# Kernel optimization log

Hardware: AMD Instinct MI355X
Metric: run time of the kernel (lower is better)

Reference implementation:

```python
import jax, jax.numpy as jnp
import numpy as np

LOG2 = 0.6931471805599453

def ssp(x):
    # ShiftedSoftplus: softplus(x) - log(2)
    return jax.nn.softplus(x) - jnp.asarray(LOG2, x.dtype)

def setup_inputs() -> dict:
    key = jax.random.key(0)
    ks = jax.random.split(key, 12)
    B, N, D, F, R, P = 1, 50000, 128, 128, 20, 1600000
    s = lambda fan_in: 1.0 / np.sqrt(fan_in)
    return {
        "x": jax.random.normal(ks[0], (B, N, D), jnp.float32),
        "f_ij": jax.random.uniform(ks[1], (P, R), jnp.float32),
        "idx_i": jax.random.randint(ks[2], (P,), 0, B * N),
        "idx_j": jax.random.randint(ks[3], (P,), 0, B * N),
        "rcut_ij": jax.random.uniform(ks[4], (P,), jnp.float32),
        "W_in": jax.random.uniform(ks[5], (F, D), jnp.float32, -s(D), s(D)),
        "b_in": jax.random.uniform(ks[6], (F,), jnp.float32, -s(D), s(D)),
        "W_filter": jax.random.uniform(ks[7], (F, R), jnp.float32, -s(R), s(R)),
        "b_filter": jax.random.uniform(ks[8], (F,), jnp.float32, -s(R), s(R)),
        "W_out": jax.random.uniform(ks[9], (D, F), jnp.float32, -s(F), s(F)),
        "b_out": jax.random.uniform(ks[10], (D,), jnp.float32, -s(F), s(F)),
    }

def reference(x, f_ij, idx_i, idx_j, rcut_ij, W_in, b_in, W_filter, b_filter, W_out, b_out):
    B, N, _ = x.shape
    # input_to_feature: Linear(nr_atom_basis -> nr_filters)
    h = jnp.einsum('bnd,fd->bnf', x, W_in) + b_in          # [B,N,F]
    h = h.reshape(B * N, -1)                                # [B*N,F]
    # filter network: Linear(nr_rbf -> nr_filters) + ShiftedSoftplus, scaled by cutoff
    Wij = ssp(jnp.einsum('pr,fr->pf', f_ij, W_filter) + b_filter) * rcut_ij[:, None]  # [P,F]
    # gather -> mul -> scatter_add
    x_ij = h[idx_j] * Wij                                   # [P,F]
    agg = jax.ops.segment_sum(x_ij, idx_i, num_segments=B * N)  # [B*N,F]
    # feature_to_output: Linear(nr_filters -> nr_atom_basis) + ShiftedSoftplus
    out = ssp(jnp.einsum('nf,df->nd', agg, W_out) + b_out)  # [B*N,D]
    return out.reshape(B, N, 128)
```

## Files before the change

kernel.cpp:

```cpp
#include <hip/hip_runtime.h>
#include <hip/hip_bf16.h>

static constexpr float kLog2 = 0.6931471805599453f;

__device__ __forceinline__ float sspf(float x) {
    return fmaxf(x, 0.0f) + __logf(1.0f + __expf(-fabsf(x))) - kLog2;
}

typedef __attribute__((ext_vector_type(8))) _Float16 half8;
typedef __attribute__((ext_vector_type(4))) _Float16 half4v;
typedef __attribute__((ext_vector_type(4))) float float4v;

template <bool ACT, typename OUT>
__device__ __forceinline__ void gemm_mfma_body(const float* __restrict__ A,
                                               const float* __restrict__ B,
                                               const float* __restrict__ bias,
                                               OUT* __restrict__ C, int M,
                                               int blockid) {
    constexpr int LDH = 136;
    __shared__ _Float16 Als[64 * LDH];
    __shared__ _Float16 Bls[128 * LDH];
    const int tid = threadIdx.x;
    const int rowbase = blockid * 64;
#pragma unroll
    for (int j = 0; j < 8; ++j) {
        int idx = j * 256 + tid;
        int r = idx >> 5, c4 = (idx & 31) << 2;
        int rg = rowbase + r;
        rg = rg < M ? rg : (M - 1);
        float4 v = *(const float4*)(A + (size_t)rg * 128 + c4);
        half4v hv = {(_Float16)v.x, (_Float16)v.y, (_Float16)v.z, (_Float16)v.w};
        *(half4v*)&Als[r * LDH + c4] = hv;
    }
#pragma unroll
    for (int j = 0; j < 16; ++j) {
        int idx = j * 256 + tid;
        int r = idx >> 5, c4 = (idx & 31) << 2;
        float4 v = *(const float4*)(B + (size_t)r * 128 + c4);
        half4v hv = {(_Float16)v.x, (_Float16)v.y, (_Float16)v.z, (_Float16)v.w};
        *(half4v*)&Bls[r * LDH + c4] = hv;
    }
    __syncthreads();

    const int wave = tid >> 6, lane = tid & 63;
    const int l15 = lane & 15, q = lane >> 4;
    float4v acc[8];
#pragma unroll
    for (int nt = 0; nt < 8; ++nt) acc[nt] = (float4v){0.f, 0.f, 0.f, 0.f};
    const int am = wave * 16 + l15;
#pragma unroll
    for (int kk = 0; kk < 4; ++kk) {
        half8 af = *(const half8*)&Als[am * LDH + kk * 32 + q * 8];
#pragma unroll
        for (int nt = 0; nt < 8; ++nt) {
            half8 bf = *(const half8*)&Bls[(nt * 16 + l15) * LDH + kk * 32 + q * 8];
            acc[nt] = __builtin_amdgcn_mfma_f32_16x16x32_f16(af, bf, acc[nt], 0, 0, 0);
        }
    }
#pragma unroll
    for (int nt = 0; nt < 8; ++nt) {
        int n = nt * 16 + l15;
        float bv = bias[n];
#pragma unroll
        for (int r = 0; r < 4; ++r) {
            int m = rowbase + wave * 16 + q * 4 + r;
            if (m < M) {
                float v = acc[nt][r] + bv;
                if (ACT) v = sspf(v);
                C[(size_t)m * 128 + n] = (OUT)v;
            }
        }
    }
}

__global__ __launch_bounds__(256) void gemm_in_count_kernel(
    const float* __restrict__ A, const float* __restrict__ B,
    const float* __restrict__ bias, _Float16* __restrict__ C, int M,
    const int* __restrict__ idx_i, int* __restrict__ counts, int P,
    int gemm_blocks) {
    if ((int)blockIdx.x < gemm_blocks) {
        gemm_mfma_body<false, _Float16>(A, B, bias, C, M, blockIdx.x);
    } else {
        const int nthr = (gridDim.x - gemm_blocks) * 256;
        for (int p = (blockIdx.x - gemm_blocks) * 256 + threadIdx.x; p < P;
             p += nthr)
            atomicAdd(&counts[idx_i[p]], 1);
    }
}

__global__ __launch_bounds__(256) void gemm_out_kernel(
    const float* __restrict__ A, const float* __restrict__ B,
    const float* __restrict__ bias, float* __restrict__ C, int M) {
    gemm_mfma_body<true, float>(A, B, bias, C, M, blockIdx.x);
}

__global__ __launch_bounds__(256) void block_sums_kernel(
    const int* __restrict__ counts, int* __restrict__ partials, int N) {
    __shared__ int red[256];
    int t = threadIdx.x, g = blockIdx.x * 256 + t;
    red[t] = g < N ? counts[g] : 0;
    __syncthreads();
    for (int o = 128; o > 0; o >>= 1) {
        if (t < o) red[t] += red[t + o];
        __syncthreads();
    }
    if (t == 0) partials[blockIdx.x] = red[0];
}

__global__ __launch_bounds__(256) void scan_partials_kernel(int* __restrict__ partials,
                                                            int NB) {
    __shared__ int s[256];
    int t = threadIdx.x;
    s[t] = t < NB ? partials[t] : 0;
    __syncthreads();
    for (int o = 1; o < 256; o <<= 1) {
        int v = t >= o ? s[t - o] : 0;
        __syncthreads();
        s[t] += v;
        __syncthreads();
    }
    partials[t] = t ? s[t - 1] : 0;
}

__global__ __launch_bounds__(256) void write_offsets_kernel(
    const int* __restrict__ counts, const int* __restrict__ partials,
    int* __restrict__ offsets, int* __restrict__ cursor, int N) {
    __shared__ int s[256];
    int t = threadIdx.x, g = blockIdx.x * 256 + t;
    int c = g < N ? counts[g] : 0;
    s[t] = c;
    __syncthreads();
    for (int o = 1; o < 256; o <<= 1) {
        int v = t >= o ? s[t - o] : 0;
        __syncthreads();
        s[t] += v;
        __syncthreads();
    }
    int excl = partials[blockIdx.x] + s[t] - c;
    if (g < N) {
        offsets[g] = excl;
        cursor[g] = excl;
        if (g == N - 1) offsets[N] = excl + c;
    }
}

__global__ __launch_bounds__(256) void fill_kernel(const int* __restrict__ idx_i,
                                                   int* __restrict__ cursor,
                                                   int* __restrict__ csr, int P) {
    int p = blockIdx.x * 256 + threadIdx.x;
    if (p < P) {
        int pos = atomicAdd(&cursor[idx_i[p]], 1);
        csr[pos] = p;
    }
}

__global__ __launch_bounds__(256) void gather_mfma_kernel(
    const float* __restrict__ f_ij, const int* __restrict__ idx_j,
    const float* __restrict__ rcut, const float* __restrict__ Wf,
    const float* __restrict__ bf, const _Float16* __restrict__ h16,
    const int* __restrict__ offsets, const int* __restrict__ csr,
    float* __restrict__ agg, int N) {
    const int lane = threadIdx.x & 63;
    const int gwave = (blockIdx.x * 256 + threadIdx.x) >> 6;
    const int nwaves = (gridDim.x * 256) >> 6;
    const int l15 = lane & 15, q = lane >> 4;

    half8 wfr[8];
#pragma unroll
    for (int nt = 0; nt < 8; ++nt) {
        const float* wr = Wf + (size_t)(nt * 16 + l15) * 20;
        float v[8];
#pragma unroll
        for (int j = 0; j < 8; ++j) {
            int k = q * 8 + j;
            v[j] = (k < 20) ? wr[k] : ((k == 20) ? bf[nt * 16 + l15] : 0.0f);
        }
        wfr[nt] = (half8){(_Float16)v[0], (_Float16)v[1], (_Float16)v[2],
                          (_Float16)v[3], (_Float16)v[4], (_Float16)v[5],
                          (_Float16)v[6], (_Float16)v[7]};
    }
    const float4v zero = {0.f, 0.f, 0.f, 0.f};

    for (int i = gwave; i < N; i += nwaves) {
        const int s = __builtin_amdgcn_readfirstlane(offsets[i]);
        const int e = __builtin_amdgcn_readfirstlane(offsets[i + 1]);
        float4v acc[8];
#pragma unroll
        for (int nt = 0; nt < 8; ++nt) acc[nt] = zero;

        for (int c = s; c < e; c += 16) {
            const int k = c + l15;
            const int pidx = k < e ? k : (e - 1);
            const int p = csr[pidx];
            const int jb = idx_j[p] << 7;
            const float rc = (k < e) ? rcut[p] : 0.0f;
            const float* fp = f_ij + (size_t)p * 20;
            float b0 = 0.f, b1 = 0.f, b2 = 0.f, b3 = 0.f;
            float b4 = 0.f, b5 = 0.f, b6 = 0.f, b7 = 0.f;
            if (q <= 2) {
                float4 a = *(const float4*)(fp + q * 8);
                b0 = a.x; b1 = a.y; b2 = a.z; b3 = a.w;
            }
            if (q <= 1) {
                float4 bb = *(const float4*)(fp + q * 8 + 4);
                b4 = bb.x; b5 = bb.y; b6 = bb.z; b7 = bb.w;
            }
            if (q == 2) b4 = 1.0f;
            half8 bfrag = (half8){(_Float16)b0, (_Float16)b1, (_Float16)b2,
                                  (_Float16)b3, (_Float16)b4, (_Float16)b5,
                                  (_Float16)b6, (_Float16)b7};
#pragma unroll
            for (int nt = 0; nt < 8; ++nt) {
                float4v d = __builtin_amdgcn_mfma_f32_16x16x32_f16(wfr[nt], bfrag,
                                                                   zero, 0, 0, 0);
                half4v hv = *(const half4v*)(h16 + jb + nt * 16 + q * 4);
#pragma unroll
                for (int r = 0; r < 4; ++r) {
                    float w = sspf(d[r]) * rc;
                    acc[nt][r] = fmaf(w, (float)hv[r], acc[nt][r]);
                }
            }
        }
#pragma unroll
        for (int m = 1; m <= 8; m <<= 1)
#pragma unroll
            for (int nt = 0; nt < 8; ++nt)
#pragma unroll
                for (int r = 0; r < 4; ++r)
                    acc[nt][r] += __shfl_xor(acc[nt][r], m, 64);
        if (l15 == 0) {
#pragma unroll
            for (int nt = 0; nt < 8; ++nt) {
                float4 o = {acc[nt][0], acc[nt][1], acc[nt][2], acc[nt][3]};
                *(float4*)(agg + (size_t)i * 128 + nt * 16 + q * 4) = o;
            }
        }
    }
}

extern "C" void kernel_launch(void* const* d_in, const int* in_sizes, int n_in,
                              void* d_out, int out_size, void* d_ws, size_t ws_size,
                              hipStream_t stream) {
    const float* x     = (const float*)d_in[0];
    const float* f_ij  = (const float*)d_in[1];
    const int*   idx_i = (const int*)d_in[2];
    const int*   idx_j = (const int*)d_in[3];
    const float* rcut  = (const float*)d_in[4];
    const float* W_in  = (const float*)d_in[5];
    const float* b_in  = (const float*)d_in[6];
    const float* W_f   = (const float*)d_in[7];
    const float* b_f   = (const float*)d_in[8];
    const float* W_out = (const float*)d_in[9];
    const float* b_out = (const float*)d_in[10];

    const int N = in_sizes[0] / 128;
    const int P = in_sizes[2];
    const int NB = (N + 255) / 256;

    char* ws = (char*)d_ws;
    int* counts   = (int*)ws;  ws += ((size_t)N + 64) * 4;
    int* offsets  = (int*)ws;  ws += ((size_t)N + 64) * 4;
    int* cursor   = (int*)ws;  ws += ((size_t)N + 64) * 4;
    int* partials = (int*)ws;  ws += 1024;
    int* csr      = (int*)ws;  ws += (size_t)P * 4;
    _Float16* h16 = (_Float16*)ws;

    float* agg = (float*)d_out;

    const int mblocks = (N + 63) / 64;
    const int cblocks = 768;

    hipMemsetAsync(counts, 0, (size_t)N * 4, stream);
    gemm_in_count_kernel<<<mblocks + cblocks, 256, 0, stream>>>(
        x, W_in, b_in, h16, N, idx_i, counts, P, mblocks);
    block_sums_kernel<<<NB, 256, 0, stream>>>(counts, partials, N);
    scan_partials_kernel<<<1, 256, 0, stream>>>(partials, NB);
    write_offsets_kernel<<<NB, 256, 0, stream>>>(counts, partials, offsets, cursor, N);
    fill_kernel<<<(P + 255) / 256, 256, 0, stream>>>(idx_i, cursor, csr, P);
    gather_mfma_kernel<<<2048, 256, 0, stream>>>(f_ij, idx_j, rcut, W_f, b_f,
                                                 h16, offsets, csr, agg, N);
    gemm_out_kernel<<<mblocks, 256, 0, stream>>>(agg, W_out, b_out, (float*)d_out, N);
}
```

Measured before the change: 765.3 us.

## Replace three-kernel scan with atomic segment allocation and pre-sorted edge features

The three-kernel prefix scan is replaced by a single kernel that scans counts within each block and reserves each block's range with an atomic on a global total. Segment starts are therefore not in node order, which is valid for CSR grouping. The fill kernel now writes the edge payload in sorted order: packed idx_j and rcut, plus fp16 f_ij padded to 24 with the bias-one column when workspace allows. The gather kernel then reads contiguous data instead of indirecting through csr into f_ij, idx_j and rcut, and it prefetches the next chunk's metadata. This trades an extra scattered write pass of about 56 bytes per edge in fill for contiguous reads in the gather.

After: 628.4 us. 17.9% less time.

```diff
diff --git a/kernel.cpp b/kernel.cpp
--- a/kernel.cpp
+++ b/kernel.cpp
@@ -53,8 +53,8 @@
         half8 af = *(const half8*)&Als[am * LDH + kk * 32 + q * 8];
 #pragma unroll
         for (int nt = 0; nt < 8; ++nt) {
-            half8 bf = *(const half8*)&Bls[(nt * 16 + l15) * LDH + kk * 32 + q * 8];
-            acc[nt] = __builtin_amdgcn_mfma_f32_16x16x32_f16(af, bf, acc[nt], 0, 0, 0);
+            half8 bfv = *(const half8*)&Bls[(nt * 16 + l15) * LDH + kk * 32 + q * 8];
+            acc[nt] = __builtin_amdgcn_mfma_f32_16x16x32_f16(af, bfv, acc[nt], 0, 0, 0);
         }
     }
 #pragma unroll
@@ -94,40 +94,13 @@
     gemm_mfma_body<true, float>(A, B, bias, C, M, blockIdx.x);
 }
 
-__global__ __launch_bounds__(256) void block_sums_kernel(
-    const int* __restrict__ counts, int* __restrict__ partials, int N) {
-    __shared__ int red[256];
-    int t = threadIdx.x, g = blockIdx.x * 256 + t;
-    red[t] = g < N ? counts[g] : 0;
-    __syncthreads();
-    for (int o = 128; o > 0; o >>= 1) {
-        if (t < o) red[t] += red[t + o];
-        __syncthreads();
-    }
-    if (t == 0) partials[blockIdx.x] = red[0];
-}
-
-__global__ __launch_bounds__(256) void scan_partials_kernel(int* __restrict__ partials,
-                                                            int NB) {
+__global__ __launch_bounds__(256) void alloc_starts_kernel(
+    const int* __restrict__ counts, int* __restrict__ starts,
+    int* __restrict__ cursor, int* __restrict__ gtot, int N) {
     __shared__ int s[256];
-    int t = threadIdx.x;
-    s[t] = t < NB ? partials[t] : 0;
-    __syncthreads();
-    for (int o = 1; o < 256; o <<= 1) {
-        int v = t >= o ? s[t - o] : 0;
-        __syncthreads();
-        s[t] += v;
-        __syncthreads();
-    }
-    partials[t] = t ? s[t - 1] : 0;
-}
-
-__global__ __launch_bounds__(256) void write_offsets_kernel(
-    const int* __restrict__ counts, const int* __restrict__ partials,
-    int* __restrict__ offsets, int* __restrict__ cursor, int N) {
-    __shared__ int s[256];
-    int t = threadIdx.x, g = blockIdx.x * 256 + t;
-    int c = g < N ? counts[g] : 0;
+    __shared__ int base;
+    const int t = threadIdx.x, g = blockIdx.x * 256 + t;
+    const int c = g < N ? counts[g] : 0;
     s[t] = c;
     __syncthreads();
     for (int o = 1; o < 256; o <<= 1) {
@@ -136,30 +109,53 @@
         s[t] += v;
         __syncthreads();
     }
-    int excl = partials[blockIdx.x] + s[t] - c;
+    if (t == 255) base = atomicAdd(gtot, s[255]);
+    __syncthreads();
+    const int excl = base + s[t] - c;
     if (g < N) {
-        offsets[g] = excl;
+        starts[g] = excl;
         cursor[g] = excl;
-        if (g == N - 1) offsets[N] = excl + c;
-    }
-}
-
-__global__ __launch_bounds__(256) void fill_kernel(const int* __restrict__ idx_i,
-                                                   int* __restrict__ cursor,
-                                                   int* __restrict__ csr, int P) {
+    }
+}
+
+template <bool EF>
+__global__ __launch_bounds__(256) void fill_kernel(
+    const int* __restrict__ idx_i, const int* __restrict__ idx_j,
+    const float* __restrict__ rcut, const float* __restrict__ f_ij,
+    int* __restrict__ cursor, _Float16* __restrict__ ef,
+    int2* __restrict__ meta, int* __restrict__ pidx, int P) {
     int p = blockIdx.x * 256 + threadIdx.x;
-    if (p < P) {
-        int pos = atomicAdd(&cursor[idx_i[p]], 1);
-        csr[pos] = p;
-    }
-}
-
+    if (p >= P) return;
+    const int i = idx_i[p];
+    const int pos = atomicAdd(&cursor[i], 1);
+    meta[pos] = make_int2(idx_j[p] << 7, __float_as_int(rcut[p]));
+    if (EF) {
+        const float* fr = f_ij + (size_t)p * 20;
+        _Float16 hb[24];
+#pragma unroll
+        for (int r = 0; r < 20; r += 4) {
+            float4 v = *(const float4*)(fr + r);
+            hb[r] = (_Float16)v.x; hb[r + 1] = (_Float16)v.y;
+            hb[r + 2] = (_Float16)v.z; hb[r + 3] = (_Float16)v.w;
+        }
+        hb[20] = (_Float16)1.0f; hb[21] = (_Float16)0.0f;
+        hb[22] = (_Float16)0.0f; hb[23] = (_Float16)0.0f;
+        _Float16* dst = ef + (size_t)pos * 24;
+        *(half8*)dst = *(half8*)hb;
+        *(half8*)(dst + 8) = *(half8*)(hb + 8);
+        *(half8*)(dst + 16) = *(half8*)(hb + 16);
+    } else {
+        pidx[pos] = p;
+    }
+}
+
+template <bool EF>
 __global__ __launch_bounds__(256) void gather_mfma_kernel(
-    const float* __restrict__ f_ij, const int* __restrict__ idx_j,
-    const float* __restrict__ rcut, const float* __restrict__ Wf,
-    const float* __restrict__ bf, const _Float16* __restrict__ h16,
-    const int* __restrict__ offsets, const int* __restrict__ csr,
-    float* __restrict__ agg, int N) {
+    const _Float16* __restrict__ ef, const int2* __restrict__ meta,
+    const int* __restrict__ pidx, const float* __restrict__ f_ij,
+    const float* __restrict__ Wf, const float* __restrict__ bf,
+    const _Float16* __restrict__ h16, const int* __restrict__ starts,
+    const int* __restrict__ counts, float* __restrict__ agg, int N) {
     const int lane = threadIdx.x & 63;
     const int gwave = (blockIdx.x * 256 + threadIdx.x) >> 6;
     const int nwaves = (gridDim.x * 256) >> 6;
@@ -182,42 +178,67 @@
     const float4v zero = {0.f, 0.f, 0.f, 0.f};
 
     for (int i = gwave; i < N; i += nwaves) {
-        const int s = __builtin_amdgcn_readfirstlane(offsets[i]);
-        const int e = __builtin_amdgcn_readfirstlane(offsets[i + 1]);
+        const int s = __builtin_amdgcn_readfirstlane(starts[i]);
+        const int cnt = __builtin_amdgcn_readfirstlane(counts[i]);
+        const int e = s + cnt;
         float4v acc[8];
 #pragma unroll
         for (int nt = 0; nt < 8; ++nt) acc[nt] = zero;
 
-        for (int c = s; c < e; c += 16) {
-            const int k = c + l15;
-            const int pidx = k < e ? k : (e - 1);
-            const int p = csr[pidx];
-            const int jb = idx_j[p] << 7;
-            const float rc = (k < e) ? rcut[p] : 0.0f;
-            const float* fp = f_ij + (size_t)p * 20;
-            float b0 = 0.f, b1 = 0.f, b2 = 0.f, b3 = 0.f;
-            float b4 = 0.f, b5 = 0.f, b6 = 0.f, b7 = 0.f;
-            if (q <= 2) {
-                float4 a = *(const float4*)(fp + q * 8);
-                b0 = a.x; b1 = a.y; b2 = a.z; b3 = a.w;
+        if (cnt > 0) {
+            int pos = min(s + l15, e - 1);
+            half8 bf_n = {};
+            if (EF) {
+                if (q < 3) bf_n = *(const half8*)(ef + (size_t)pos * 24 + q * 8);
             }
-            if (q <= 1) {
-                float4 bb = *(const float4*)(fp + q * 8 + 4);
-                b4 = bb.x; b5 = bb.y; b6 = bb.z; b7 = bb.w;
-            }
-            if (q == 2) b4 = 1.0f;
-            half8 bfrag = (half8){(_Float16)b0, (_Float16)b1, (_Float16)b2,
-                                  (_Float16)b3, (_Float16)b4, (_Float16)b5,
-                                  (_Float16)b6, (_Float16)b7};
-#pragma unroll
-            for (int nt = 0; nt < 8; ++nt) {
-                float4v d = __builtin_amdgcn_mfma_f32_16x16x32_f16(wfr[nt], bfrag,
-                                                                   zero, 0, 0, 0);
-                half4v hv = *(const half4v*)(h16 + jb + nt * 16 + q * 4);
-#pragma unroll
-                for (int r = 0; r < 4; ++r) {
-                    float w = sspf(d[r]) * rc;
-                    acc[nt][r] = fmaf(w, (float)hv[r], acc[nt][r]);
+            int2 mt_n = meta[pos];
+            int p_n = EF ? 0 : pidx[pos];
+
+            for (int c = s; c < e; c += 16) {
+                half8 bf_c = bf_n;
+                int2 mt_c = mt_n;
+                int p_c = p_n;
+                if (c + 16 < e) {
+                    int np = min(c + 16 + l15, e - 1);
+                    if (EF) {
+                        if (q < 3) bf_n = *(const half8*)(ef + (size_t)np * 24 + q * 8);
+                    } else {
+                        p_n = pidx[np];
+                    }
+                    mt_n = meta[np];
+                }
+                if (!EF) {
+                    const float* fp = f_ij + (size_t)p_c * 20;
+                    float b0 = 0.f, b1 = 0.f, b2 = 0.f, b3 = 0.f;
+                    float b4 = 0.f, b5 = 0.f, b6 = 0.f, b7 = 0.f;
+                    if (q <= 2) {
+                        float4 a = *(const float4*)(fp + q * 8);
+                        b0 = a.x; b1 = a.y; b2 = a.z; b3 = a.w;
+                    }
+                    if (q <= 1) {
+                        float4 bb = *(const float4*)(fp + q * 8 + 4);
+                        b4 = bb.x; b5 = bb.y; b6 = bb.z; b7 = bb.w;
+                    }
+                    if (q == 2) b4 = 1.0f;
+                    bf_c = (half8){(_Float16)b0, (_Float16)b1, (_Float16)b2,
+                                   (_Float16)b3, (_Float16)b4, (_Float16)b5,
+                                   (_Float16)b6, (_Float16)b7};
+                }
+                const int jb = mt_c.x;
+                const float rc = (c + l15 < e) ? __int_as_float(mt_c.y) : 0.0f;
+                half4v hv[8];
+#pragma unroll
+                for (int nt = 0; nt < 8; ++nt)
+                    hv[nt] = *(const half4v*)(h16 + jb + nt * 16 + q * 4);
+#pragma unroll
+                for (int nt = 0; nt < 8; ++nt) {
+                    float4v d = __builtin_amdgcn_mfma_f32_16x16x32_f16(
+                        wfr[nt], bf_c, zero, 0, 0, 0);
+#pragma unroll
+                    for (int r = 0; r < 4; ++r) {
+                        float w = sspf(d[r]) * rc;
+                        acc[nt][r] = fmaf(w, (float)hv[nt][r], acc[nt][r]);
+                    }
                 }
             }
         }
@@ -255,29 +276,47 @@
 
     const int N = in_sizes[0] / 128;
     const int P = in_sizes[2];
-    const int NB = (N + 255) / 256;
 
     char* ws = (char*)d_ws;
-    int* counts   = (int*)ws;  ws += ((size_t)N + 64) * 4;
-    int* offsets  = (int*)ws;  ws += ((size_t)N + 64) * 4;
-    int* cursor   = (int*)ws;  ws += ((size_t)N + 64) * 4;
-    int* partials = (int*)ws;  ws += 1024;
-    int* csr      = (int*)ws;  ws += (size_t)P * 4;
-    _Float16* h16 = (_Float16*)ws;
+    size_t off = 0;
+    auto alloc = [&](size_t bytes) {
+        void* ptr = ws + off;
+        off += (bytes + 15) & ~(size_t)15;
+        return ptr;
+    };
+    int* counts  = (int*)alloc((size_t)N * 4 + 16);
+    int* gtot    = counts + N;
+    int* starts  = (int*)alloc((size_t)N * 4);
+    int* cursor  = (int*)alloc((size_t)N * 4);
+    _Float16* h16 = (_Float16*)alloc((size_t)N * 128 * 2);
+    int2* meta   = (int2*)alloc((size_t)P * 8);
+    size_t base_need = off;
+    const bool use_ef = (base_need + (size_t)P * 24 * 2 + 64) <= ws_size;
+    _Float16* ef = nullptr;
+    int* pidx = nullptr;
+    if (use_ef) ef = (_Float16*)alloc((size_t)P * 24 * 2 + 64);
+    else        pidx = (int*)alloc((size_t)P * 4);
 
     float* agg = (float*)d_out;
 
     const int mblocks = (N + 63) / 64;
     const int cblocks = 768;
-
-    hipMemsetAsync(counts, 0, (size_t)N * 4, stream);
+    const int NB = (N + 255) / 256;
+
+    hipMemsetAsync(counts, 0, (size_t)N * 4 + 16, stream);
     gemm_in_count_kernel<<<mblocks + cblocks, 256, 0, stream>>>(
         x, W_in, b_in, h16, N, idx_i, counts, P, mblocks);
-    block_sums_kernel<<<NB, 256, 0, stream>>>(counts, partials, N);
-    scan_partials_kernel<<<1, 256, 0, stream>>>(partials, NB);
-    write_offsets_kernel<<<NB, 256, 0, stream>>>(counts, partials, offsets, cursor, N);
-    fill_kernel<<<(P + 255) / 256, 256, 0, stream>>>(idx_i, cursor, csr, P);
-    gather_mfma_kernel<<<2048, 256, 0, stream>>>(f_ij, idx_j, rcut, W_f, b_f,
-                                                 h16, offsets, csr, agg, N);
+    alloc_starts_kernel<<<NB, 256, 0, stream>>>(counts, starts, cursor, gtot, N);
+    if (use_ef) {
+        fill_kernel<true><<<(P + 255) / 256, 256, 0, stream>>>(
+            idx_i, idx_j, rcut, f_ij, cursor, ef, meta, pidx, P);
+        gather_mfma_kernel<true><<<2048, 256, 0, stream>>>(
+            ef, meta, pidx, f_ij, W_f, b_f, h16, starts, counts, agg, N);
+    } else {
+        fill_kernel<false><<<(P + 255) / 256, 256, 0, stream>>>(
+            idx_i, idx_j, rcut, f_ij, cursor, ef, meta, pidx, P);
+        gather_mfma_kernel<false><<<2048, 256, 0, stream>>>(
+            ef, meta, pidx, f_ij, W_f, b_f, h16, starts, counts, agg, N);
+    }
     gemm_out_kernel<<<mblocks, 256, 0, stream>>>(agg, W_out, b_out, (float*)d_out, N);
 }
```
